# Optimization experiments

Hardware: AMD Instinct MI355X
Metric: run time of the kernel (lower is better)

The kernel has to match this reference:

```python
import jax, jax.numpy as jnp
import numpy as np

B, CIN, COUT, DIM_IN, K, H, W = 16, 256, 256, 32, 3, 128, 128
GROUPS = 1
ICG = CIN // GROUPS


def setup_inputs() -> dict:
    key = jax.random.key(0)
    ks = jax.random.split(key, 10)
    s = 0.02
    return {
        "base_x": jax.random.normal(ks[0], (B, CIN, H, W), dtype=jnp.float32),
        "tran_x": jax.random.normal(ks[1], (B, DIM_IN), dtype=jnp.float32),
        # g2pa_wgen MLP: Linear(dim_in+in, out) -> ReLU -> Linear(out, 16) -> ReLU -> Linear(16, in//g + out + k^2)
        "mlp_w1": jax.random.normal(ks[2], (COUT, DIM_IN + CIN), dtype=jnp.float32) * s,
        "mlp_b1": jnp.zeros((COUT,), dtype=jnp.float32),
        "mlp_w2": jax.random.normal(ks[3], (16, COUT), dtype=jnp.float32) * s,
        "mlp_b2": jnp.zeros((16,), dtype=jnp.float32),
        "mlp_w3": jax.random.normal(ks[4], (ICG + COUT + K * K, 16), dtype=jnp.float32) * s,
        "mlp_b3": jnp.zeros((ICG + COUT + K * K,), dtype=jnp.float32),
        # base conv params
        "conv_w": jax.random.normal(ks[5], (COUT, ICG, K, K), dtype=jnp.float32) * s,
        "conv_b": jnp.zeros((COUT,), dtype=jnp.float32),
    }


def reference(base_x, tran_x, mlp_w1, mlp_b1, mlp_w2, mlp_b2, mlp_w3, mlp_b3, conv_w, conv_b):
    b = base_x.shape[0]
    # global average pool of base_x -> [B, CIN]
    in_x = jnp.mean(base_x, axis=(-2, -1))
    # small MLP generating attention logits
    h = jnp.concatenate([tran_x, in_x], axis=-1)
    h = jax.nn.relu(h @ mlp_w1.T + mlp_b1)
    h = jax.nn.relu(h @ mlp_w2.T + mlp_b2)
    att_raw = h @ mlp_w3.T + mlp_b3  # [B, COUT + ICG + K^2]
    w1 = att_raw[:, :COUT]                         # [B, COUT]
    w2 = att_raw[:, COUT:COUT + ICG]               # [B, ICG]
    w3 = att_raw[:, COUT + ICG:]                   # [B, K^2]
    # outer-product sigmoid attention: [B, ICG, COUT]
    att = jax.nn.sigmoid(w1[:, None, :] + w2[:, :, None])
    # scale by spatial logits and softmax over k^2: [B, ICG, COUT, K^2]
    att = att[..., None] * w3[:, None, None, :]
    att = jax.nn.softmax(att, axis=-1)
    # torch .view memory reinterpretation [B,ICG,COUT,K^2] -> [B,COUT,ICG,K,K]
    att = att.reshape(b, COUT, ICG, K, K) * (K * K)
    # per-sample modulated conv weights
    eff_w = conv_w[None] * att  # [B, COUT, ICG, K, K]

    def conv1(x, w):
        # x: [CIN,H,W], w: [COUT,ICG,K,K]
        y = jax.lax.conv_general_dilated(
            x[None], w, window_strides=(1, 1), padding=((1, 1), (1, 1)),
            dimension_numbers=("NCHW", "OIHW", "NCHW"))
        return y[0]

    out = jax.vmap(conv1)(base_x, eff_w) + conv_b[None, :, None, None]
    return out
```

## Files before the change

kernel.cpp:

```cpp
#include <hip/hip_runtime.h>

#define HH 128
#define WW 128
#define CI 256
#define CO 256

typedef __attribute__((ext_vector_type(8))) short short8;
typedef __attribute__((ext_vector_type(4))) float f32x4;

__device__ inline unsigned short f2b(float f) {
    unsigned int u = __builtin_bit_cast(unsigned int, f);
    unsigned int r = (u + 0x7FFFu + ((u >> 16) & 1u)) >> 16;
    return (unsigned short)r;
}

__global__ __launch_bounds__(256) void k_prep(const float* __restrict__ bx,
                                              unsigned short* __restrict__ xT,
                                              float* __restrict__ in_sum) {
    const int cchunk = blockIdx.x;
    const int y      = blockIdx.y;
    const int b      = blockIdx.z;
    const int t      = threadIdx.x;

    __shared__ unsigned short tile[32 * 128];
    __shared__ float psums[4][256];

    const float* src = bx + ((size_t)(b * CI + cchunk * 32) * HH + y) * WW;

#pragma unroll
    for (int r = 0; r < 4; ++r) {
        int cl = r * 8 + (t >> 5);
        int x  = (t & 31) * 4;
        float4 v = *(const float4*)(src + (size_t)cl * HH * WW + x);
        unsigned int lo = (unsigned int)f2b(v.x) | ((unsigned int)f2b(v.y) << 16);
        unsigned int hi = (unsigned int)f2b(v.z) | ((unsigned int)f2b(v.w) << 16);
        *(uint2*)(&tile[cl * 128 + x]) = make_uint2(lo, hi);
        psums[r][t] = v.x + v.y + v.z + v.w;
    }
    __syncthreads();

    if (t < 32) {
        float s = 0.f;
#pragma unroll
        for (int j = 0; j < 32; ++j) s += psums[t >> 3][(t & 7) * 32 + j];
        atomicAdd(&in_sum[b * CI + cchunk * 32 + t], s);
    }

    unsigned short* dst = xT + ((size_t)(b * HH + y) * WW) * 256 + cchunk * 32;
#pragma unroll
    for (int r = 0; r < 2; ++r) {
        int idx = r * 256 + t;
        int x   = idx >> 2;
        int cc  = (idx & 3) * 8;
        int4 pk;
        unsigned short* vp = reinterpret_cast<unsigned short*>(&pk);
#pragma unroll
        for (int j = 0; j < 8; ++j) vp[j] = tile[(cc + j) * 128 + x];
        *(int4*)(dst + (size_t)x * 256 + cc) = pk;
    }
}

__global__ __launch_bounds__(256) void k_mlp(const float* __restrict__ tran,
                                             const float* __restrict__ in_sum,
                                             const float* __restrict__ w1, const float* __restrict__ b1,
                                             const float* __restrict__ w2, const float* __restrict__ b2,
                                             const float* __restrict__ w3, const float* __restrict__ b3,
                                             float* __restrict__ attr) {
    const int b = blockIdx.x;
    const int t = threadIdx.x;
    __shared__ float cat[288];
    __shared__ float h1[256];
    __shared__ float h2[16];

    if (t < 32) cat[t] = tran[b * 32 + t];
    cat[32 + t] = in_sum[b * 256 + t] * (1.f / 16384.f);
    __syncthreads();

    float a1 = b1[t];
    for (int i = 0; i < 288; ++i) a1 += cat[i] * w1[t * 288 + i];
    h1[t] = fmaxf(a1, 0.f);
    __syncthreads();

    if (t < 16) {
        float a2 = b2[t];
        for (int j = 0; j < 256; ++j) a2 += h1[j] * w2[t * 256 + j];
        h2[t] = fmaxf(a2, 0.f);
    }
    __syncthreads();

    for (int r = t; r < 521; r += 256) {
        float a3 = b3[r];
#pragma unroll
        for (int j = 0; j < 16; ++j) a3 += h2[j] * w3[r * 16 + j];
        attr[b * 521 + r] = a3;
    }
}

__global__ __launch_bounds__(256) void k_effw(const float* __restrict__ attr,
                                              const float* __restrict__ conv_w,
                                              unsigned short* __restrict__ weff) {
    const int P = blockIdx.x;
    const int b = blockIdx.y;
    const int q = threadIdx.x;
    const float* ar = attr + b * 521;

    float s = ar[q] + ar[256 + P];
    s = 1.f / (1.f + expf(-s));

    float lg[9];
    float m = -1e30f;
#pragma unroll
    for (int k = 0; k < 9; ++k) { lg[k] = ar[512 + k] * s; m = fmaxf(m, lg[k]); }
    float e[9];
    float sum = 0.f;
#pragma unroll
    for (int k = 0; k < 9; ++k) { e[k] = expf(lg[k] - m); sum += e[k]; }
    float scale = 9.f / sum;

    const float* cw = conv_w + ((size_t)P * 256 + q) * 9;
#pragma unroll
    for (int tap = 0; tap < 9; ++tap) {
        float w = cw[tap] * e[tap] * scale;
        weff[((size_t)(b * 9 + tap) * 256 + P) * 256 + q] = f2b(w);
    }
}

__global__ __launch_bounds__(256) void k_conv(const unsigned short* __restrict__ xT,
                                              const unsigned short* __restrict__ weff,
                                              const float* __restrict__ conv_b,
                                              float* __restrict__ out) {
    const int tile = blockIdx.x;
    const int P0   = blockIdx.y * 128;
    const int b    = blockIdx.z;
    const int ty = tile >> 3, tx = tile & 7;
    const int y0 = ty * 8, x0 = tx * 16;

    const int t    = threadIdx.x;
    const int lane = t & 63;
    const int wid  = t >> 6;
    const int wr = wid >> 1, wc = wid & 1;
    const int ln15 = lane & 15, kb = lane >> 4;

    __shared__ __align__(16) unsigned char lds[180 * 80];

    f32x4 acc[4][4];
#pragma unroll
    for (int i = 0; i < 4; ++i)
#pragma unroll
        for (int j = 0; j < 4; ++j) acc[i][j] = f32x4{0.f, 0.f, 0.f, 0.f};

    const unsigned short* xb = xT + (size_t)b * HH * WW * 256;
    const unsigned short* wb = weff + (size_t)b * 9 * 65536
                             + (size_t)(P0 + wr * 64 + ln15) * 256 + (kb << 3);

    for (int qc = 0; qc < 256; qc += 32) {
        __syncthreads();
        for (int idx = t; idx < 720; idx += 256) {
            int pos = idx >> 2, ch = idx & 3;
            int py = pos / 18, px = pos - py * 18;
            int gy = y0 - 1 + py, gx = x0 - 1 + px;
            int4 v = {0, 0, 0, 0};
            if ((unsigned)gy < 128u && (unsigned)gx < 128u)
                v = *(const int4*)(xb + (((size_t)gy * 128 + gx) * 256 + qc + ch * 8));
            *(int4*)(lds + pos * 80 + ch * 16) = v;
        }
        __syncthreads();

#pragma unroll
        for (int tap = 0; tap < 9; ++tap) {
            const int dy = tap / 3, dx = tap % 3;
            const unsigned short* wp = wb + (size_t)tap * 65536 + qc;
            short8 a[4];
#pragma unroll
            for (int mi = 0; mi < 4; ++mi)
                a[mi] = *(const short8*)(wp + mi * 16 * 256);
            short8 bf[4];
#pragma unroll
            for (int ni = 0; ni < 4; ++ni) {
                int pos = (wc * 4 + ni + dy) * 18 + ln15 + dx;
                bf[ni] = *(const short8*)(lds + pos * 80 + (kb << 4));
            }
#pragma unroll
            for (int mi = 0; mi < 4; ++mi)
#pragma unroll
                for (int ni = 0; ni < 4; ++ni)
                    acc[mi][ni] = __builtin_amdgcn_mfma_f32_16x16x32_bf16(
                        a[mi], bf[ni], acc[mi][ni], 0, 0, 0);
        }
    }

#pragma unroll
    for (int mi = 0; mi < 4; ++mi) {
        int pbase = P0 + wr * 64 + mi * 16 + kb * 4;
#pragma unroll
        for (int r = 0; r < 4; ++r) {
            float bias = conv_b[pbase + r];
#pragma unroll
            for (int ni = 0; ni < 4; ++ni) {
                int yy = y0 + wc * 4 + ni;
                out[(((size_t)b * 256 + pbase + r) * 128 + yy) * 128 + x0 + ln15] =
                    acc[mi][ni][r] + bias;
            }
        }
    }
}

extern "C" void kernel_launch(void* const* d_in, const int* in_sizes, int n_in,
                              void* d_out, int out_size, void* d_ws, size_t ws_size,
                              hipStream_t stream) {
    const float* base_x = (const float*)d_in[0];
    const float* tran_x = (const float*)d_in[1];
    const float* w1     = (const float*)d_in[2];
    const float* b1     = (const float*)d_in[3];
    const float* w2     = (const float*)d_in[4];
    const float* b2     = (const float*)d_in[5];
    const float* w3     = (const float*)d_in[6];
    const float* b3     = (const float*)d_in[7];
    const float* conv_w = (const float*)d_in[8];
    const float* conv_b = (const float*)d_in[9];
    float* out = (float*)d_out;

    char* ws = (char*)d_ws;
    unsigned short* xT   = (unsigned short*)(ws);
    unsigned short* weff = (unsigned short*)(ws + 134217728);
    float* attr          = (float*)(ws + 153092096);
    float* in_sum        = (float*)(ws + 153125440);

    hipMemsetAsync(in_sum, 0, 16 * 256 * sizeof(float), stream);

    k_prep<<<dim3(8, 128, 16), 256, 0, stream>>>(base_x, xT, in_sum);
    k_mlp<<<16, 256, 0, stream>>>(tran_x, in_sum, w1, b1, w2, b2, w3, b3, attr);
    k_effw<<<dim3(256, 16), 256, 0, stream>>>(attr, conv_w, weff);
    k_conv<<<dim3(128, 2, 16), 256, 0, stream>>>(xT, weff, conv_b, out);
}
```

Baseline: 1.192 ms.

## Pad input, double-buffer conv LDS via direct global-to-LDS loads, prefetch weights

The input is now stored with a zero halo, so the conv kernel can load tiles with global_load_lds directly into LDS without bounds checks. A double-buffered LDS stage overlaps the next channel chunk's load with the current chunk's MFMAs, and weight fragments are prefetched two taps ahead in a rotating register set. Blocks are remapped with a swizzled linear index, occupancy is set through launch bounds, and k_effw stages conv_w in shared memory. Costs include an extra zeroing kernel, more registers, and an unpadded LDS layout with a 64-byte stride that may cause bank conflicts.

Result: faster. 1.103 ms (-7.5%).

```diff
diff --git a/kernel.cpp b/kernel.cpp
--- a/kernel.cpp
+++ b/kernel.cpp
@@ -2,8 +2,7 @@
 
 #define HH 128
 #define WW 128
-#define CI 256
-#define CO 256
+#define PW 130
 
 typedef __attribute__((ext_vector_type(8))) short short8;
 typedef __attribute__((ext_vector_type(4))) float f32x4;
@@ -14,8 +13,31 @@
     return (unsigned short)r;
 }
 
+__device__ inline void g2l16(const unsigned short* g, unsigned short* l) {
+    __builtin_amdgcn_global_load_lds(
+        (const __attribute__((address_space(1))) unsigned int*)g,
+        (__attribute__((address_space(3))) unsigned int*)(unsigned int)(size_t)l,
+        16, 0, 0);
+}
+
+__global__ __launch_bounds__(256) void k_zero(unsigned short* __restrict__ xpad) {
+    const int b = blockIdx.x;
+    const int t = threadIdx.x;
+    for (int i = t; i < 516; i += 256) {
+        int y, x;
+        if (i < 130)      { y = 0;           x = i; }
+        else if (i < 260) { y = 129;         x = i - 130; }
+        else if (i < 388) { y = i - 260 + 1; x = 0; }
+        else              { y = i - 388 + 1; x = 129; }
+        int4* p = (int4*)(xpad + ((size_t)(b * PW + y) * PW + x) * 256);
+        int4 z = {0, 0, 0, 0};
+#pragma unroll
+        for (int j = 0; j < 32; ++j) p[j] = z;
+    }
+}
+
 __global__ __launch_bounds__(256) void k_prep(const float* __restrict__ bx,
-                                              unsigned short* __restrict__ xT,
+                                              unsigned short* __restrict__ xpad,
                                               float* __restrict__ in_sum) {
     const int cchunk = blockIdx.x;
     const int y      = blockIdx.y;
@@ -25,7 +47,7 @@
     __shared__ unsigned short tile[32 * 128];
     __shared__ float psums[4][256];
 
-    const float* src = bx + ((size_t)(b * CI + cchunk * 32) * HH + y) * WW;
+    const float* src = bx + ((size_t)(b * 256 + cchunk * 32) * HH + y) * WW;
 
 #pragma unroll
     for (int r = 0; r < 4; ++r) {
@@ -43,10 +65,10 @@
         float s = 0.f;
 #pragma unroll
         for (int j = 0; j < 32; ++j) s += psums[t >> 3][(t & 7) * 32 + j];
-        atomicAdd(&in_sum[b * CI + cchunk * 32 + t], s);
-    }
-
-    unsigned short* dst = xT + ((size_t)(b * HH + y) * WW) * 256 + cchunk * 32;
+        atomicAdd(&in_sum[b * 256 + cchunk * 32 + t], s);
+    }
+
+    unsigned short* dst = xpad + ((size_t)(b * PW + y + 1) * PW + 1) * 256 + cchunk * 32;
 #pragma unroll
     for (int r = 0; r < 2; ++r) {
         int idx = r * 256 + t;
@@ -102,8 +124,11 @@
     const int P = blockIdx.x;
     const int b = blockIdx.y;
     const int q = threadIdx.x;
+
+    __shared__ float cw[2304];
+    for (int i = q; i < 2304; i += 256) cw[i] = conv_w[(size_t)P * 2304 + i];
+
     const float* ar = attr + b * 521;
-
     float s = ar[q] + ar[256 + P];
     s = 1.f / (1.f + expf(-s));
 
@@ -116,32 +141,43 @@
 #pragma unroll
     for (int k = 0; k < 9; ++k) { e[k] = expf(lg[k] - m); sum += e[k]; }
     float scale = 9.f / sum;
-
-    const float* cw = conv_w + ((size_t)P * 256 + q) * 9;
+    __syncthreads();
+
 #pragma unroll
     for (int tap = 0; tap < 9; ++tap) {
-        float w = cw[tap] * e[tap] * scale;
+        float w = cw[q * 9 + tap] * e[tap] * scale;
         weff[((size_t)(b * 9 + tap) * 256 + P) * 256 + q] = f2b(w);
     }
 }
 
-__global__ __launch_bounds__(256) void k_conv(const unsigned short* __restrict__ xT,
-                                              const unsigned short* __restrict__ weff,
-                                              const float* __restrict__ conv_b,
-                                              float* __restrict__ out) {
-    const int tile = blockIdx.x;
-    const int P0   = blockIdx.y * 128;
-    const int b    = blockIdx.z;
+__global__ __launch_bounds__(256, 3) void k_conv(const unsigned short* __restrict__ xpad,
+                                                 const unsigned short* __restrict__ weff,
+                                                 const float* __restrict__ conv_b,
+                                                 float* __restrict__ out) {
+    const int raw = blockIdx.x;
+    const int lin = (raw & 7) * 512 + (raw >> 3);
+    const int tile = lin & 127;
+    const int P0   = ((lin >> 7) & 1) * 128;
+    const int b    = lin >> 8;
     const int ty = tile >> 3, tx = tile & 7;
     const int y0 = ty * 8, x0 = tx * 16;
 
     const int t    = threadIdx.x;
     const int lane = t & 63;
-    const int wid  = t >> 6;
-    const int wr = wid >> 1, wc = wid & 1;
+    const int w    = t >> 6;
+    const int wr = w >> 1, wc = w & 1;
     const int ln15 = lane & 15, kb = lane >> 4;
 
-    __shared__ __align__(16) unsigned char lds[180 * 80];
+    __shared__ __align__(16) unsigned char lds[2][12288];
+
+    int goff[3];
+#pragma unroll
+    for (int j = 0; j < 3; ++j) {
+        int c16 = (w * 3 + j) * 16 + (lane >> 2);
+        int pos = c16 < 180 ? c16 : 0;
+        int py = pos / 18, px = pos - py * 18;
+        goff[j] = ((b * PW + y0 + py) * PW + x0 + px) * 256 + (lane & 3) * 8;
+    }
 
     f32x4 acc[4][4];
 #pragma unroll
@@ -149,44 +185,53 @@
 #pragma unroll
         for (int j = 0; j < 4; ++j) acc[i][j] = f32x4{0.f, 0.f, 0.f, 0.f};
 
-    const unsigned short* xb = xT + (size_t)b * HH * WW * 256;
     const unsigned short* wb = weff + (size_t)b * 9 * 65536
                              + (size_t)(P0 + wr * 64 + ln15) * 256 + (kb << 3);
 
-    for (int qc = 0; qc < 256; qc += 32) {
-        __syncthreads();
-        for (int idx = t; idx < 720; idx += 256) {
-            int pos = idx >> 2, ch = idx & 3;
-            int py = pos / 18, px = pos - py * 18;
-            int gy = y0 - 1 + py, gx = x0 - 1 + px;
-            int4 v = {0, 0, 0, 0};
-            if ((unsigned)gy < 128u && (unsigned)gx < 128u)
-                v = *(const int4*)(xb + (((size_t)gy * 128 + gx) * 256 + qc + ch * 8));
-            *(int4*)(lds + pos * 80 + ch * 16) = v;
+    short8 a[3][4];
+
+    auto stage = [&](int buf, int qc) {
+#pragma unroll
+        for (int j = 0; j < 3; ++j)
+            g2l16(xpad + goff[j] + qc, (unsigned short*)&lds[buf][(w * 3 + j) * 1024]);
+    };
+    auto issueA = [&](int slot, int tap, int qc) {
+#pragma unroll
+        for (int mi = 0; mi < 4; ++mi)
+            a[slot][mi] = *(const short8*)(wb + tap * 65536 + qc + mi * 4096);
+    };
+
+    stage(0, 0);
+    issueA(0, 0, 0);
+    issueA(1, 1, 0);
+    __syncthreads();
+
+    int cur = 0;
+    for (int s = 0; s < 8; ++s) {
+        const int qc = s * 32;
+        if (s < 7) stage(cur ^ 1, qc + 32);
+
+#pragma unroll
+        for (int tap = 0; tap < 9; ++tap) {
+            if (tap < 7)      issueA((tap + 2) % 3, tap + 2, qc);
+            else if (s < 7)   issueA((tap + 2) % 3, tap - 7, qc + 32);
+
+            const int dy = tap / 3, dx = tap - dy * 3;
+            short8 bf[4];
+#pragma unroll
+            for (int ni = 0; ni < 4; ++ni) {
+                int pos = (wc * 4 + ni + dy) * 18 + ln15 + dx;
+                bf[ni] = *(const short8*)(&lds[cur][pos * 64 + (kb << 4)]);
+            }
+#pragma unroll
+            for (int mi = 0; mi < 4; ++mi)
+#pragma unroll
+                for (int ni = 0; ni < 4; ++ni)
+                    acc[mi][ni] = __builtin_amdgcn_mfma_f32_16x16x32_bf16(
+                        a[tap % 3][mi], bf[ni], acc[mi][ni], 0, 0, 0);
         }
         __syncthreads();
-
-#pragma unroll
-        for (int tap = 0; tap < 9; ++tap) {
-            const int dy = tap / 3, dx = tap % 3;
-            const unsigned short* wp = wb + (size_t)tap * 65536 + qc;
-            short8 a[4];
-#pragma unroll
-            for (int mi = 0; mi < 4; ++mi)
-                a[mi] = *(const short8*)(wp + mi * 16 * 256);
-            short8 bf[4];
-#pragma unroll
-            for (int ni = 0; ni < 4; ++ni) {
-                int pos = (wc * 4 + ni + dy) * 18 + ln15 + dx;
-                bf[ni] = *(const short8*)(lds + pos * 80 + (kb << 4));
-            }
-#pragma unroll
-            for (int mi = 0; mi < 4; ++mi)
-#pragma unroll
-                for (int ni = 0; ni < 4; ++ni)
-                    acc[mi][ni] = __builtin_amdgcn_mfma_f32_16x16x32_bf16(
-                        a[mi], bf[ni], acc[mi][ni], 0, 0, 0);
-        }
+        cur ^= 1;
     }
 
 #pragma unroll
@@ -221,15 +266,16 @@
     float* out = (float*)d_out;
 
     char* ws = (char*)d_ws;
-    unsigned short* xT   = (unsigned short*)(ws);
-    unsigned short* weff = (unsigned short*)(ws + 134217728);
-    float* attr          = (float*)(ws + 153092096);
-    float* in_sum        = (float*)(ws + 153125440);
+    unsigned short* xpad = (unsigned short*)(ws);
+    unsigned short* weff = (unsigned short*)(ws + 138444800);
+    float* attr          = (float*)(ws + 157319168);
+    float* in_sum        = (float*)(ws + 157352512);
 
     hipMemsetAsync(in_sum, 0, 16 * 256 * sizeof(float), stream);
 
-    k_prep<<<dim3(8, 128, 16), 256, 0, stream>>>(base_x, xT, in_sum);
+    k_zero<<<16, 256, 0, stream>>>(xpad);
+    k_prep<<<dim3(8, 128, 16), 256, 0, stream>>>(base_x, xpad, in_sum);
     k_mlp<<<16, 256, 0, stream>>>(tran_x, in_sum, w1, b1, w2, b2, w3, b3, attr);
     k_effw<<<dim3(256, 16), 256, 0, stream>>>(attr, conv_w, weff);
-    k_conv<<<dim3(128, 2, 16), 256, 0, stream>>>(xT, weff, conv_b, out);
-}
+    k_conv<<<4096, 256, 0, stream>>>(xpad, weff, conv_b, out);
+}
```
